# Performance work log

Hardware: AMD Instinct MI355X
Metric: run time of the kernel (lower is better)

The kernel has to match this reference:

```python
import jax, jax.numpy as jnp
import numpy as np

WS = 8      # window_size
NH = 4      # num_heads
DM = 128    # d_model
DK = DM // NH


def _rel_pos_index(ws):
    # matches compute_relative_position_index (static, numpy)
    coords = np.stack(np.meshgrid(np.arange(ws), np.arange(ws), indexing='ij'))  # (2,ws,ws)
    cf = coords.reshape(2, -1)                       # (2, ws*ws)
    rel = (cf[:, :, None] - cf[:, None, :]).transpose(1, 2, 0)  # (S,S,2)
    rel[..., 0] += ws - 1
    rel[..., 1] += ws - 1
    rel[..., 0] *= 2 * ws - 1
    return rel.sum(-1)                               # (S,S) int


def _attn_mask(H, W, ws, ss):
    # matches create_attention_mask (static, numpy)
    row = np.broadcast_to(np.arange(H)[:, None], (H, W))
    col = np.broadcast_to(np.arange(W)[None, :], (H, W))
    wid = row // ws * (W // ws) + col // ws
    wid = np.roll(wid, (-ss, -ss), axis=(0, 1))
    wid = wid.reshape(H // ws, ws, W // ws, ws).transpose(0, 2, 1, 3).reshape(-1, ws * ws)
    return (wid[:, :, None] != wid[:, None, :]).astype(np.float32) * -100.0  # (nw,S,S)


def setup_inputs() -> dict:
    key = jax.random.key(0)
    ks = jax.random.split(key, 10)
    B, N = 16, 128 * 128
    w = lambda k, s: jax.random.normal(k, s, jnp.float32) * 0.02
    return {
        "x": jax.random.normal(ks[0], (B, N, DM), jnp.float32),
        "wq": w(ks[1], (DM, DM)), "bq": jnp.zeros((DM,), jnp.float32),
        "wk": w(ks[2], (DM, DM)), "bk": jnp.zeros((DM,), jnp.float32),
        "wv": w(ks[3], (DM, DM)), "bv": jnp.zeros((DM,), jnp.float32),
        "wo": w(ks[4], (DM, DM)), "bo": jnp.zeros((DM,), jnp.float32),
        "bias_table": w(ks[5], ((2 * WS - 1) ** 2, NH)),
        "shift": 1,
    }


def reference(x, wq, bq, wk, bk, wv, bv, wo, bo, bias_table, shift):
    B, N, C = x.shape
    H = W = int(round(N ** 0.5))
    S = WS * WS
    nw_h, nw_w = H // WS, W // WS
    nw = nw_h * nw_w

    # relative position bias: (NH, S, S)
    rel_idx = _rel_pos_index(WS).reshape(-1)
    bias = bias_table[rel_idx].reshape(S, S, NH).transpose(2, 0, 1)

    xi = x.reshape(B, H, W, C)
    if shift:
        xi = jnp.roll(xi, ((-WS) // 2, (-WS) // 2), axis=(1, 2))

    # window partition -> (B*nw, S, C)
    xw = xi.reshape(B, nw_h, WS, nw_w, WS, C).transpose(0, 1, 3, 2, 4, 5).reshape(B * nw, S, C)

    def proj(w_, b_):
        return (xw @ w_ + b_).reshape(B * nw, S, NH, DK).transpose(0, 2, 1, 3)  # (Bn,NH,S,DK)

    q, k, v = proj(wq, bq), proj(wk, bk), proj(wv, bv)

    scores = jnp.einsum('bhnd,bhmd->bhnm', q, k) / jnp.sqrt(jnp.float32(DK))
    if shift:
        mask = jnp.asarray(_attn_mask(H, W, WS, WS // 2))  # (nw,S,S)
        scores = (scores.reshape(B, nw, NH, S, S) + mask[None, :, None]).reshape(B * nw, NH, S, S)
    scores = scores + bias[None]

    attn = jax.nn.softmax(scores, axis=-1)
    out = jnp.einsum('bhnm,bhmd->bhnd', attn, v)          # (Bn,NH,S,DK)
    out = out.transpose(0, 2, 1, 3).reshape(B * nw, S, DM)
    return out @ wo + bo                                   # (B*nw, S, DM)
```

## Files before the change

### kernel.cpp

```cpp
#include <hip/hip_runtime.h>


typedef __attribute__((ext_vector_type(8))) short bf16x8;
typedef __attribute__((ext_vector_type(4))) float f32x4;

#define MFMA16(a, b, c) __builtin_amdgcn_mfma_f32_16x16x32_bf16((a), (b), (c), 0, 0, 0)

__device__ __forceinline__ unsigned short f2bf(float f) {
  union { float f; unsigned int u; } v; v.f = f;
  unsigned int r = v.u + 0x7fffu + ((v.u >> 16) & 1u);
  return (unsigned short)(r >> 16);
}

__device__ __forceinline__ bf16x8 pack8(f32x4 a, f32x4 b) {
  bf16x8 r;
  r[0] = (short)f2bf(a[0]); r[1] = (short)f2bf(a[1]);
  r[2] = (short)f2bf(a[2]); r[3] = (short)f2bf(a[3]);
  r[4] = (short)f2bf(b[0]); r[5] = (short)f2bf(b[1]);
  r[6] = (short)f2bf(b[2]); r[7] = (short)f2bf(b[3]);
  return r;
}

__global__ void prep_kernel(const float* __restrict__ wq, const float* __restrict__ wk,
                            const float* __restrict__ wv, const float* __restrict__ wo,
                            const float* __restrict__ bias_table,
                            unsigned short* __restrict__ wt, float* __restrict__ bias_full) {
  int tid = blockIdx.x * 256 + threadIdx.x;
  int m = tid >> 14, idx = tid & 16383;
  int n = idx >> 7, k = idx & 127;
  const float* w = (m == 0) ? wq : (m == 1) ? wk : (m == 2) ? wv : wo;
  wt[m * 16384 + n * 128 + k] = f2bf(w[k * 128 + n]);
  if (tid < 16384) {
    int h = tid >> 12, r = tid & 4095;
    int s1 = r >> 6, s2 = r & 63;
    int rel = ((s1 >> 3) - (s2 >> 3) + 7) * 15 + ((s1 & 7) - (s2 & 7) + 7);
    bias_full[tid] = bias_table[rel * 4 + h];
  }
}

__global__ __launch_bounds__(256, 3) void winattn_kernel(
    const float* __restrict__ x,
    const float* __restrict__ bq, const float* __restrict__ bk,
    const float* __restrict__ bv, const float* __restrict__ bo,
    const unsigned short* __restrict__ wt,
    const float* __restrict__ bias_full,
    const int* __restrict__ shiftp,
    float* __restrict__ out) {
  __shared__ __align__(16) char smem[16384];
  const int tid = threadIdx.x;
  const int h = tid >> 6, lane = tid & 63;
  const int g = lane >> 4, c16 = lane & 15;
  const int win = blockIdx.x;
  const int bb = win >> 8, widx = win & 255;
  const int wh = widx >> 4, ww = widx & 15;
  const int shift = shiftp[0];
  const int ss = shift ? 4 : 0;

#pragma unroll
  for (int it = 0; it < 4; ++it) {
    int cid = tid + it * 256;
    int s = cid >> 4, cc = (cid & 15) << 3;
    int r0 = (wh * 8 + (s >> 3) + ss) & 127;
    int c0 = (ww * 8 + (s & 7) + ss) & 127;
    const float* src = x + ((bb * 16384 + r0 * 128 + c0) * 128 + cc);
    float4 lo = *(const float4*)src;
    float4 hi = *(const float4*)(src + 4);
    bf16x8 v;
    v[0] = (short)f2bf(lo.x); v[1] = (short)f2bf(lo.y);
    v[2] = (short)f2bf(lo.z); v[3] = (short)f2bf(lo.w);
    v[4] = (short)f2bf(hi.x); v[5] = (short)f2bf(hi.y);
    v[6] = (short)f2bf(hi.z); v[7] = (short)f2bf(hi.w);
    *(bf16x8*)(smem + s * 256 + ((cc * 2) ^ ((s & 7) << 4))) = v;
  }
  __syncthreads();

  const f32x4 z4 = {0.f, 0.f, 0.f, 0.f};

  f32x4 qacc[2][4], kacc[2][4], vacc[4][2];
#pragma unroll
  for (int i = 0; i < 4; ++i) {
    qacc[0][i] = z4; qacc[1][i] = z4;
    kacc[0][i] = z4; kacc[1][i] = z4;
    vacc[i][0] = z4; vacc[i][1] = z4;
  }
  const unsigned short* wq_ = wt + (h * 32 + c16) * 128;
  const unsigned short* wk_ = wt + 16384 + (h * 32 + c16) * 128;
  const unsigned short* wv_ = wt + 32768 + (h * 32 + c16) * 128;
#pragma unroll
  for (int kk = 0; kk < 4; ++kk) {
    const int co = kk * 32 + g * 8;
    bf16x8 xfr[4];
#pragma unroll
    for (int t = 0; t < 4; ++t) {
      int row = t * 16 + c16;
      xfr[t] = *(const bf16x8*)(smem + row * 256 + ((co * 2) ^ ((row & 7) << 4)));
    }
    bf16x8 wqf0 = *(const bf16x8*)(wq_ + co);
    bf16x8 wqf1 = *(const bf16x8*)(wq_ + 2048 + co);
    bf16x8 wkf0 = *(const bf16x8*)(wk_ + co);
    bf16x8 wkf1 = *(const bf16x8*)(wk_ + 2048 + co);
    bf16x8 wvf0 = *(const bf16x8*)(wv_ + co);
    bf16x8 wvf1 = *(const bf16x8*)(wv_ + 2048 + co);
#pragma unroll
    for (int t = 0; t < 4; ++t) {
      qacc[0][t] = MFMA16(wqf0, xfr[t], qacc[0][t]);
      qacc[1][t] = MFMA16(wqf1, xfr[t], qacc[1][t]);
      kacc[0][t] = MFMA16(wkf0, xfr[t], kacc[0][t]);
      kacc[1][t] = MFMA16(wkf1, xfr[t], kacc[1][t]);
      vacc[t][0] = MFMA16(xfr[t], wvf0, vacc[t][0]);
      vacc[t][1] = MFMA16(xfr[t], wvf1, vacc[t][1]);
    }
  }

  bf16x8 qb16[4], kb16[4], vb16[2][2];
  {
    const float scale = 0.17677669529663687f;
    f32x4 bq4[2], bk4[2];
    bq4[0] = *(const f32x4*)(bq + h * 32 + g * 4);
    bq4[1] = *(const f32x4*)(bq + h * 32 + 16 + g * 4);
    bk4[0] = *(const f32x4*)(bk + h * 32 + g * 4);
    bk4[1] = *(const f32x4*)(bk + h * 32 + 16 + g * 4);
#pragma unroll
    for (int t = 0; t < 4; ++t) {
      f32x4 q0, q1, k0, k1;
#pragma unroll
      for (int r = 0; r < 4; ++r) {
        q0[r] = (qacc[0][t][r] + bq4[0][r]) * scale;
        q1[r] = (qacc[1][t][r] + bq4[1][r]) * scale;
        k0[r] = kacc[0][t][r] + bk4[0][r];
        k1[r] = kacc[1][t][r] + bk4[1][r];
      }
      qb16[t] = pack8(q0, q1);
      kb16[t] = pack8(k0, k1);
    }
    float bv0 = bv[h * 32 + c16];
    float bv1 = bv[h * 32 + 16 + c16];
#pragma unroll
    for (int ks = 0; ks < 2; ++ks) {
      f32x4 v00, v10, v01, v11;
#pragma unroll
      for (int r = 0; r < 4; ++r) {
        v00[r] = vacc[2 * ks][0][r] + bv0;
        v10[r] = vacc[2 * ks + 1][0][r] + bv0;
        v01[r] = vacc[2 * ks][1][r] + bv1;
        v11[r] = vacc[2 * ks + 1][1][r] + bv1;
      }
      vb16[ks][0] = pack8(v00, v10);
      vb16[ks][1] = pack8(v01, v11);
    }
  }

  f32x4 sc[4][4];
#pragma unroll
  for (int a = 0; a < 4; ++a)
#pragma unroll
    for (int b = 0; b < 4; ++b) sc[a][b] = MFMA16(kb16[a], qb16[b], z4);

  int w1i[4] = {0, 0, 0, 0};
  int w2i[4][4] = {};
  if (shift) {
#pragma unroll
    for (int b = 0; b < 4; ++b) {
      int s1 = b * 16 + c16;
      int r0 = (wh * 8 + (s1 >> 3) + ss) & 127;
      int c0 = (ww * 8 + (s1 & 7) + ss) & 127;
      w1i[b] = (r0 >> 3) * 16 + (c0 >> 3);
    }
#pragma unroll
    for (int a = 0; a < 4; ++a)
#pragma unroll
      for (int r = 0; r < 4; ++r) {
        int s2 = a * 16 + g * 4 + r;
        int r0 = (wh * 8 + (s2 >> 3) + ss) & 127;
        int c0 = (ww * 8 + (s2 & 7) + ss) & 127;
        w2i[a][r] = (r0 >> 3) * 16 + (c0 >> 3);
      }
  }

  bf16x8 pa[4][2];
  const float* bfh = bias_full + h * 4096 + c16 * 64 + g * 4;
#pragma unroll
  for (int b = 0; b < 4; ++b) {
    const float* bfr = bfh + b * 1024;
    f32x4 bia[4];
#pragma unroll
    for (int a = 0; a < 4; ++a) bia[a] = *(const f32x4*)(bfr + a * 16);
    float mx = -1e30f;
#pragma unroll
    for (int a = 0; a < 4; ++a)
#pragma unroll
      for (int r = 0; r < 4; ++r) {
        float v = sc[a][b][r] + bia[a][r];
        if (shift && (w1i[b] != w2i[a][r])) v -= 100.f;
        sc[a][b][r] = v;
        mx = fmaxf(mx, v);
      }
    mx = fmaxf(mx, __shfl_xor(mx, 16));
    mx = fmaxf(mx, __shfl_xor(mx, 32));
    float sum = 0.f;
#pragma unroll
    for (int a = 0; a < 4; ++a)
#pragma unroll
      for (int r = 0; r < 4; ++r) {
        float e = __expf(sc[a][b][r] - mx);
        sc[a][b][r] = e;
        sum += e;
      }
    sum += __shfl_xor(sum, 16);
    sum += __shfl_xor(sum, 32);
    float inv = 1.0f / sum;
#pragma unroll
    for (int a = 0; a < 4; ++a)
#pragma unroll
      for (int r = 0; r < 4; ++r) sc[a][b][r] *= inv;
    pa[b][0] = pack8(sc[0][b], sc[1][b]);
    pa[b][1] = pack8(sc[2][b], sc[3][b]);
  }

  f32x4 o[4][2];
#pragma unroll
  for (int b = 0; b < 4; ++b) { o[b][0] = z4; o[b][1] = z4; }
#pragma unroll
  for (int b = 0; b < 4; ++b)
#pragma unroll
    for (int ks = 0; ks < 2; ++ks) {
      o[b][0] = MFMA16(pa[b][ks], vb16[ks][0], o[b][0]);
      o[b][1] = MFMA16(pa[b][ks], vb16[ks][1], o[b][1]);
    }

  __syncthreads();

#pragma unroll
  for (int b = 0; b < 4; ++b)
#pragma unroll
    for (int nt = 0; nt < 2; ++nt)
#pragma unroll
      for (int r = 0; r < 4; ++r) {
        int row = b * 16 + g * 4 + r;
        int col = h * 32 + nt * 16 + c16;
        *(unsigned short*)(smem + row * 256 + ((col * 2) ^ ((row & 7) << 4))) =
            f2bf(o[b][nt][r]);
      }
  __syncthreads();

  {
    f32x4 acc[8];
#pragma unroll
    for (int nt = 0; nt < 8; ++nt) acc[nt] = z4;
    const int arow = h * 16 + c16;
    const int asw = (arow & 7) << 4;
#pragma unroll
    for (int kk = 0; kk < 4; ++kk) {
      const int co = kk * 32 + g * 8;
      bf16x8 a = *(const bf16x8*)(smem + arow * 256 + ((co * 2) ^ asw));
#pragma unroll
      for (int nt = 0; nt < 8; ++nt) {
        bf16x8 bfr = *(const bf16x8*)(wt + 49152 + (nt * 16 + c16) * 128 + co);
        acc[nt] = MFMA16(a, bfr, acc[nt]);
      }
    }
#pragma unroll
    for (int nt = 0; nt < 8; ++nt) {
      int n = nt * 16 + c16;
      float bn = bo[n];
#pragma unroll
      for (int r = 0; r < 4; ++r) {
        int row = h * 16 + g * 4 + r;
        out[(size_t)win * 8192 + (size_t)(row * 128 + n)] = acc[nt][r] + bn;
      }
    }
  }
}

extern "C" void kernel_launch(void* const* d_in, const int* in_sizes, int n_in,
                              void* d_out, int out_size, void* d_ws, size_t ws_size,
                              hipStream_t stream) {
  const float* x = (const float*)d_in[0];
  const float* wq = (const float*)d_in[1];
  const float* bq = (const float*)d_in[2];
  const float* wk = (const float*)d_in[3];
  const float* bk = (const float*)d_in[4];
  const float* wv = (const float*)d_in[5];
  const float* bv = (const float*)d_in[6];
  const float* wo = (const float*)d_in[7];
  const float* bo = (const float*)d_in[8];
  const float* bias_table = (const float*)d_in[9];
  const int* shiftp = (const int*)d_in[10];

  unsigned short* wt = (unsigned short*)d_ws;
  float* bias_full = (float*)((char*)d_ws + 131072);

  prep_kernel<<<256, 256, 0, stream>>>(wq, wk, wv, wo, bias_table, wt, bias_full);
  winattn_kernel<<<4096, 256, 0, stream>>>(x, bq, bk, bv, bo, wt, bias_full, shiftp,
                                           (float*)d_out);
}
```

Measured before the change: 190.9 us.

## Process two windows per block with register-prefetched next window input

Each block now handles two windows, starting the global loads of the second window's input into registers while the first window's attention runs, then converting and storing them into a separate LDS region. This aims to hide global load latency behind compute. It also uses the hardware packed bf16 convert instruction, folds log2(e) into the Q scale and bias table so softmax can use exp2, and raises launch bounds to 4 blocks per CU. The cost is twice the LDS per block, extra live registers for the prefetch, and half as many blocks in the grid.

```diff
diff --git a/kernel.cpp b/kernel.cpp
--- a/kernel.cpp
+++ b/kernel.cpp
@@ -5,20 +5,31 @@
 typedef __attribute__((ext_vector_type(4))) float f32x4;
 
 #define MFMA16(a, b, c) __builtin_amdgcn_mfma_f32_16x16x32_bf16((a), (b), (c), 0, 0, 0)
-
-__device__ __forceinline__ unsigned short f2bf(float f) {
-  union { float f; unsigned int u; } v; v.f = f;
-  unsigned int r = v.u + 0x7fffu + ((v.u >> 16) & 1u);
-  return (unsigned short)(r >> 16);
-}
-
+#define EXP2F(x) __builtin_amdgcn_exp2f(x)
+
+#define XW_OFF 0
+#define STG_OFF 16384
+#define LDS_BYTES 32768
+
+__device__ __forceinline__ unsigned int cvt_pk(float lo, float hi) {
+  unsigned int r;
+  asm("v_cvt_pk_bf16_f32 %0, %1, %2" : "=v"(r) : "v"(lo), "v"(hi));
+  return r;
+}
+__device__ __forceinline__ unsigned short f2bf1(float f) {
+  return (unsigned short)(cvt_pk(f, f) & 0xffffu);
+}
 __device__ __forceinline__ bf16x8 pack8(f32x4 a, f32x4 b) {
-  bf16x8 r;
-  r[0] = (short)f2bf(a[0]); r[1] = (short)f2bf(a[1]);
-  r[2] = (short)f2bf(a[2]); r[3] = (short)f2bf(a[3]);
-  r[4] = (short)f2bf(b[0]); r[5] = (short)f2bf(b[1]);
-  r[6] = (short)f2bf(b[2]); r[7] = (short)f2bf(b[3]);
-  return r;
+  union { unsigned int w[4]; bf16x8 v; } u;
+  u.w[0] = cvt_pk(a[0], a[1]); u.w[1] = cvt_pk(a[2], a[3]);
+  u.w[2] = cvt_pk(b[0], b[1]); u.w[3] = cvt_pk(b[2], b[3]);
+  return u.v;
+}
+__device__ __forceinline__ bf16x8 packf4(float4 lo, float4 hi) {
+  union { unsigned int w[4]; bf16x8 v; } u;
+  u.w[0] = cvt_pk(lo.x, lo.y); u.w[1] = cvt_pk(lo.z, lo.w);
+  u.w[2] = cvt_pk(hi.x, hi.y); u.w[3] = cvt_pk(hi.z, hi.w);
+  return u.v;
 }
 
 __global__ void prep_kernel(const float* __restrict__ wq, const float* __restrict__ wk,
@@ -29,16 +40,28 @@
   int m = tid >> 14, idx = tid & 16383;
   int n = idx >> 7, k = idx & 127;
   const float* w = (m == 0) ? wq : (m == 1) ? wk : (m == 2) ? wv : wo;
-  wt[m * 16384 + n * 128 + k] = f2bf(w[k * 128 + n]);
+  wt[m * 16384 + n * 128 + k] = f2bf1(w[k * 128 + n]);
   if (tid < 16384) {
     int h = tid >> 12, r = tid & 4095;
     int s1 = r >> 6, s2 = r & 63;
     int rel = ((s1 >> 3) - (s2 >> 3) + 7) * 15 + ((s1 & 7) - (s2 & 7) + 7);
-    bias_full[tid] = bias_table[rel * 4 + h];
+    bias_full[tid] = bias_table[rel * 4 + h] * 1.4426950408889634f;
   }
 }
 
-__global__ __launch_bounds__(256, 3) void winattn_kernel(
+__device__ __forceinline__ const float* gsrc(const float* __restrict__ x, int bb, int wh,
+                                             int ww, int ss, int cid) {
+  int s = cid >> 4, cc = (cid & 15) << 3;
+  int r0 = (wh * 8 + (s >> 3) + ss) & 127;
+  int c0 = (ww * 8 + (s & 7) + ss) & 127;
+  return x + ((bb * 16384 + r0 * 128 + c0) * 128 + cc);
+}
+__device__ __forceinline__ void store_xw(char* smem, int cid, bf16x8 v) {
+  int s = cid >> 4, cc = (cid & 15) << 3;
+  *(bf16x8*)(smem + XW_OFF + s * 256 + ((cc * 2) ^ ((s & 7) << 4))) = v;
+}
+
+__global__ __launch_bounds__(256, 4) void winattn_kernel(
     const float* __restrict__ x,
     const float* __restrict__ bq, const float* __restrict__ bk,
     const float* __restrict__ bv, const float* __restrict__ bo,
@@ -46,227 +69,255 @@
     const float* __restrict__ bias_full,
     const int* __restrict__ shiftp,
     float* __restrict__ out) {
-  __shared__ __align__(16) char smem[16384];
+  __shared__ __align__(16) char smem[LDS_BYTES];
   const int tid = threadIdx.x;
   const int h = tid >> 6, lane = tid & 63;
   const int g = lane >> 4, c16 = lane & 15;
-  const int win = blockIdx.x;
-  const int bb = win >> 8, widx = win & 255;
-  const int wh = widx >> 4, ww = widx & 15;
   const int shift = shiftp[0];
   const int ss = shift ? 4 : 0;
-
-#pragma unroll
-  for (int it = 0; it < 4; ++it) {
-    int cid = tid + it * 256;
-    int s = cid >> 4, cc = (cid & 15) << 3;
-    int r0 = (wh * 8 + (s >> 3) + ss) & 127;
-    int c0 = (ww * 8 + (s & 7) + ss) & 127;
-    const float* src = x + ((bb * 16384 + r0 * 128 + c0) * 128 + cc);
-    float4 lo = *(const float4*)src;
-    float4 hi = *(const float4*)(src + 4);
-    bf16x8 v;
-    v[0] = (short)f2bf(lo.x); v[1] = (short)f2bf(lo.y);
-    v[2] = (short)f2bf(lo.z); v[3] = (short)f2bf(lo.w);
-    v[4] = (short)f2bf(hi.x); v[5] = (short)f2bf(hi.y);
-    v[6] = (short)f2bf(hi.z); v[7] = (short)f2bf(hi.w);
-    *(bf16x8*)(smem + s * 256 + ((cc * 2) ^ ((s & 7) << 4))) = v;
+  const f32x4 z4 = {0.f, 0.f, 0.f, 0.f};
+
+  const int win0 = blockIdx.x, win1 = blockIdx.x + 2048;
+  const int bb1 = win1 >> 8, wh1 = (win1 >> 4) & 15, ww1 = win1 & 15;
+
+  {
+    const int bb0 = win0 >> 8, wh0 = (win0 >> 4) & 15, ww0 = win0 & 15;
+#pragma unroll
+    for (int it = 0; it < 4; ++it) {
+      int cid = tid + it * 256;
+      const float* src = gsrc(x, bb0, wh0, ww0, ss, cid);
+      float4 lo = *(const float4*)src;
+      float4 hi = *(const float4*)(src + 4);
+      store_xw(smem, cid, packf4(lo, hi));
+    }
   }
-  __syncthreads();
-
-  const f32x4 z4 = {0.f, 0.f, 0.f, 0.f};
-
-  f32x4 qacc[2][4], kacc[2][4], vacc[4][2];
-#pragma unroll
-  for (int i = 0; i < 4; ++i) {
-    qacc[0][i] = z4; qacc[1][i] = z4;
-    kacc[0][i] = z4; kacc[1][i] = z4;
-    vacc[i][0] = z4; vacc[i][1] = z4;
+  float4 pre0[4], pre1[4];
+  {
+    const float* s0 = gsrc(x, bb1, wh1, ww1, ss, tid);
+    const float* s1 = gsrc(x, bb1, wh1, ww1, ss, tid + 256);
+    pre0[0] = *(const float4*)s0; pre0[1] = *(const float4*)(s0 + 4);
+    pre0[2] = *(const float4*)s1; pre0[3] = *(const float4*)(s1 + 4);
   }
-  const unsigned short* wq_ = wt + (h * 32 + c16) * 128;
-  const unsigned short* wk_ = wt + 16384 + (h * 32 + c16) * 128;
-  const unsigned short* wv_ = wt + 32768 + (h * 32 + c16) * 128;
-#pragma unroll
-  for (int kk = 0; kk < 4; ++kk) {
-    const int co = kk * 32 + g * 8;
-    bf16x8 xfr[4];
-#pragma unroll
-    for (int t = 0; t < 4; ++t) {
-      int row = t * 16 + c16;
-      xfr[t] = *(const bf16x8*)(smem + row * 256 + ((co * 2) ^ ((row & 7) << 4)));
-    }
-    bf16x8 wqf0 = *(const bf16x8*)(wq_ + co);
-    bf16x8 wqf1 = *(const bf16x8*)(wq_ + 2048 + co);
-    bf16x8 wkf0 = *(const bf16x8*)(wk_ + co);
-    bf16x8 wkf1 = *(const bf16x8*)(wk_ + 2048 + co);
-    bf16x8 wvf0 = *(const bf16x8*)(wv_ + co);
-    bf16x8 wvf1 = *(const bf16x8*)(wv_ + 2048 + co);
-#pragma unroll
-    for (int t = 0; t < 4; ++t) {
-      qacc[0][t] = MFMA16(wqf0, xfr[t], qacc[0][t]);
-      qacc[1][t] = MFMA16(wqf1, xfr[t], qacc[1][t]);
-      kacc[0][t] = MFMA16(wkf0, xfr[t], kacc[0][t]);
-      kacc[1][t] = MFMA16(wkf1, xfr[t], kacc[1][t]);
-      vacc[t][0] = MFMA16(xfr[t], wvf0, vacc[t][0]);
-      vacc[t][1] = MFMA16(xfr[t], wvf1, vacc[t][1]);
-    }
-  }
-
-  bf16x8 qb16[4], kb16[4], vb16[2][2];
-  {
-    const float scale = 0.17677669529663687f;
-    f32x4 bq4[2], bk4[2];
-    bq4[0] = *(const f32x4*)(bq + h * 32 + g * 4);
-    bq4[1] = *(const f32x4*)(bq + h * 32 + 16 + g * 4);
-    bk4[0] = *(const f32x4*)(bk + h * 32 + g * 4);
-    bk4[1] = *(const f32x4*)(bk + h * 32 + 16 + g * 4);
-#pragma unroll
-    for (int t = 0; t < 4; ++t) {
-      f32x4 q0, q1, k0, k1;
-#pragma unroll
-      for (int r = 0; r < 4; ++r) {
-        q0[r] = (qacc[0][t][r] + bq4[0][r]) * scale;
-        q1[r] = (qacc[1][t][r] + bq4[1][r]) * scale;
-        k0[r] = kacc[0][t][r] + bk4[0][r];
-        k1[r] = kacc[1][t][r] + bk4[1][r];
-      }
-      qb16[t] = pack8(q0, q1);
-      kb16[t] = pack8(k0, k1);
-    }
-    float bv0 = bv[h * 32 + c16];
-    float bv1 = bv[h * 32 + 16 + c16];
-#pragma unroll
-    for (int ks = 0; ks < 2; ++ks) {
-      f32x4 v00, v10, v01, v11;
-#pragma unroll
-      for (int r = 0; r < 4; ++r) {
-        v00[r] = vacc[2 * ks][0][r] + bv0;
-        v10[r] = vacc[2 * ks + 1][0][r] + bv0;
-        v01[r] = vacc[2 * ks][1][r] + bv1;
-        v11[r] = vacc[2 * ks + 1][1][r] + bv1;
-      }
-      vb16[ks][0] = pack8(v00, v10);
-      vb16[ks][1] = pack8(v01, v11);
-    }
-  }
-
-  f32x4 sc[4][4];
-#pragma unroll
-  for (int a = 0; a < 4; ++a)
-#pragma unroll
-    for (int b = 0; b < 4; ++b) sc[a][b] = MFMA16(kb16[a], qb16[b], z4);
-
-  int w1i[4] = {0, 0, 0, 0};
-  int w2i[4][4] = {};
-  if (shift) {
-#pragma unroll
-    for (int b = 0; b < 4; ++b) {
-      int s1 = b * 16 + c16;
-      int r0 = (wh * 8 + (s1 >> 3) + ss) & 127;
-      int c0 = (ww * 8 + (s1 & 7) + ss) & 127;
-      w1i[b] = (r0 >> 3) * 16 + (c0 >> 3);
-    }
-#pragma unroll
-    for (int a = 0; a < 4; ++a)
-#pragma unroll
-      for (int r = 0; r < 4; ++r) {
-        int s2 = a * 16 + g * 4 + r;
-        int r0 = (wh * 8 + (s2 >> 3) + ss) & 127;
-        int c0 = (ww * 8 + (s2 & 7) + ss) & 127;
-        w2i[a][r] = (r0 >> 3) * 16 + (c0 >> 3);
-      }
-  }
-
-  bf16x8 pa[4][2];
-  const float* bfh = bias_full + h * 4096 + c16 * 64 + g * 4;
-#pragma unroll
-  for (int b = 0; b < 4; ++b) {
-    const float* bfr = bfh + b * 1024;
-    f32x4 bia[4];
-#pragma unroll
-    for (int a = 0; a < 4; ++a) bia[a] = *(const f32x4*)(bfr + a * 16);
-    float mx = -1e30f;
-#pragma unroll
-    for (int a = 0; a < 4; ++a)
-#pragma unroll
-      for (int r = 0; r < 4; ++r) {
-        float v = sc[a][b][r] + bia[a][r];
-        if (shift && (w1i[b] != w2i[a][r])) v -= 100.f;
-        sc[a][b][r] = v;
-        mx = fmaxf(mx, v);
-      }
-    mx = fmaxf(mx, __shfl_xor(mx, 16));
-    mx = fmaxf(mx, __shfl_xor(mx, 32));
-    float sum = 0.f;
-#pragma unroll
-    for (int a = 0; a < 4; ++a)
-#pragma unroll
-      for (int r = 0; r < 4; ++r) {
-        float e = __expf(sc[a][b][r] - mx);
-        sc[a][b][r] = e;
-        sum += e;
-      }
-    sum += __shfl_xor(sum, 16);
-    sum += __shfl_xor(sum, 32);
-    float inv = 1.0f / sum;
-#pragma unroll
-    for (int a = 0; a < 4; ++a)
-#pragma unroll
-      for (int r = 0; r < 4; ++r) sc[a][b][r] *= inv;
-    pa[b][0] = pack8(sc[0][b], sc[1][b]);
-    pa[b][1] = pack8(sc[2][b], sc[3][b]);
-  }
-
-  f32x4 o[4][2];
-#pragma unroll
-  for (int b = 0; b < 4; ++b) { o[b][0] = z4; o[b][1] = z4; }
-#pragma unroll
-  for (int b = 0; b < 4; ++b)
-#pragma unroll
-    for (int ks = 0; ks < 2; ++ks) {
-      o[b][0] = MFMA16(pa[b][ks], vb16[ks][0], o[b][0]);
-      o[b][1] = MFMA16(pa[b][ks], vb16[ks][1], o[b][1]);
-    }
-
-  __syncthreads();
-
-#pragma unroll
-  for (int b = 0; b < 4; ++b)
-#pragma unroll
-    for (int nt = 0; nt < 2; ++nt)
-#pragma unroll
-      for (int r = 0; r < 4; ++r) {
-        int row = b * 16 + g * 4 + r;
-        int col = h * 32 + nt * 16 + c16;
-        *(unsigned short*)(smem + row * 256 + ((col * 2) ^ ((row & 7) << 4))) =
-            f2bf(o[b][nt][r]);
-      }
-  __syncthreads();
-
-  {
-    f32x4 acc[8];
-#pragma unroll
-    for (int nt = 0; nt < 8; ++nt) acc[nt] = z4;
-    const int arow = h * 16 + c16;
-    const int asw = (arow & 7) << 4;
+
+  for (int w = 0; w < 2; ++w) {
+    const int win = w ? win1 : win0;
+    const int wh = (win >> 4) & 15, ww = win & 15;
+    __syncthreads();
+
+    f32x4 qacc[2][4], kacc[2][4], vacc[4][2];
+#pragma unroll
+    for (int i = 0; i < 4; ++i) {
+      qacc[0][i] = z4; qacc[1][i] = z4;
+      kacc[0][i] = z4; kacc[1][i] = z4;
+      vacc[i][0] = z4; vacc[i][1] = z4;
+    }
+    const unsigned short* wq_ = wt + (h * 32 + c16) * 128;
+    const unsigned short* wk_ = wt + 16384 + (h * 32 + c16) * 128;
+    const unsigned short* wv_ = wt + 32768 + (h * 32 + c16) * 128;
 #pragma unroll
     for (int kk = 0; kk < 4; ++kk) {
       const int co = kk * 32 + g * 8;
-      bf16x8 a = *(const bf16x8*)(smem + arow * 256 + ((co * 2) ^ asw));
+      bf16x8 xfr[4];
+#pragma unroll
+      for (int t = 0; t < 4; ++t) {
+        int row = t * 16 + c16;
+        xfr[t] = *(const bf16x8*)(smem + XW_OFF + row * 256 + ((co * 2) ^ ((row & 7) << 4)));
+      }
+      bf16x8 wqf0 = *(const bf16x8*)(wq_ + co);
+      bf16x8 wqf1 = *(const bf16x8*)(wq_ + 2048 + co);
+      bf16x8 wkf0 = *(const bf16x8*)(wk_ + co);
+      bf16x8 wkf1 = *(const bf16x8*)(wk_ + 2048 + co);
+      bf16x8 wvf0 = *(const bf16x8*)(wv_ + co);
+      bf16x8 wvf1 = *(const bf16x8*)(wv_ + 2048 + co);
+#pragma unroll
+      for (int t = 0; t < 4; ++t) {
+        qacc[0][t] = MFMA16(wqf0, xfr[t], qacc[0][t]);
+        qacc[1][t] = MFMA16(wqf1, xfr[t], qacc[1][t]);
+        kacc[0][t] = MFMA16(wkf0, xfr[t], kacc[0][t]);
+        kacc[1][t] = MFMA16(wkf1, xfr[t], kacc[1][t]);
+        vacc[t][0] = MFMA16(xfr[t], wvf0, vacc[t][0]);
+        vacc[t][1] = MFMA16(xfr[t], wvf1, vacc[t][1]);
+      }
+    }
+
+    bf16x8 qb16[4], kb16[4], vb16[2][2];
+    {
+      const float scale = 0.17677669529663687f * 1.4426950408889634f;
+      f32x4 bq4[2], bk4[2];
+      bq4[0] = *(const f32x4*)(bq + h * 32 + g * 4);
+      bq4[1] = *(const f32x4*)(bq + h * 32 + 16 + g * 4);
+      bk4[0] = *(const f32x4*)(bk + h * 32 + g * 4);
+      bk4[1] = *(const f32x4*)(bk + h * 32 + 16 + g * 4);
+#pragma unroll
+      for (int t = 0; t < 4; ++t) {
+        f32x4 q0, q1, k0, k1;
+#pragma unroll
+        for (int r = 0; r < 4; ++r) {
+          q0[r] = (qacc[0][t][r] + bq4[0][r]) * scale;
+          q1[r] = (qacc[1][t][r] + bq4[1][r]) * scale;
+          k0[r] = kacc[0][t][r] + bk4[0][r];
+          k1[r] = kacc[1][t][r] + bk4[1][r];
+        }
+        qb16[t] = pack8(q0, q1);
+        kb16[t] = pack8(k0, k1);
+      }
+      float bv0 = bv[h * 32 + c16];
+      float bv1 = bv[h * 32 + 16 + c16];
+#pragma unroll
+      for (int ks = 0; ks < 2; ++ks) {
+        f32x4 v00, v10, v01, v11;
+#pragma unroll
+        for (int r = 0; r < 4; ++r) {
+          v00[r] = vacc[2 * ks][0][r] + bv0;
+          v10[r] = vacc[2 * ks + 1][0][r] + bv0;
+          v01[r] = vacc[2 * ks][1][r] + bv1;
+          v11[r] = vacc[2 * ks + 1][1][r] + bv1;
+        }
+        vb16[ks][0] = pack8(v00, v10);
+        vb16[ks][1] = pack8(v01, v11);
+      }
+    }
+
+    f32x4 sc[4][4];
+#pragma unroll
+    for (int a = 0; a < 4; ++a)
+#pragma unroll
+      for (int b = 0; b < 4; ++b) sc[a][b] = MFMA16(kb16[a], qb16[b], z4);
+
+    int w1i[4] = {0, 0, 0, 0};
+    int w2i[4][4] = {};
+    if (shift) {
+#pragma unroll
+      for (int b = 0; b < 4; ++b) {
+        int s1 = b * 16 + c16;
+        int r0 = (wh * 8 + (s1 >> 3) + ss) & 127;
+        int c0 = (ww * 8 + (s1 & 7) + ss) & 127;
+        w1i[b] = (r0 >> 3) * 16 + (c0 >> 3);
+      }
+#pragma unroll
+      for (int a = 0; a < 4; ++a)
+#pragma unroll
+        for (int r = 0; r < 4; ++r) {
+          int s2 = a * 16 + g * 4 + r;
+          int r0 = (wh * 8 + (s2 >> 3) + ss) & 127;
+          int c0 = (ww * 8 + (s2 & 7) + ss) & 127;
+          w2i[a][r] = (r0 >> 3) * 16 + (c0 >> 3);
+        }
+    }
+
+    bf16x8 pa[4][2];
+    const float* bfh = bias_full + h * 4096 + c16 * 64 + g * 4;
+#pragma unroll
+    for (int b = 0; b < 4; ++b) {
+      const float* bfr = bfh + b * 1024;
+      f32x4 bia[4];
+#pragma unroll
+      for (int a = 0; a < 4; ++a) bia[a] = *(const f32x4*)(bfr + a * 16);
+#pragma unroll
+      for (int a = 0; a < 4; ++a)
+#pragma unroll
+        for (int r = 0; r < 4; ++r) {
+          float v = sc[a][b][r] + bia[a][r];
+          if (shift && (w1i[b] != w2i[a][r])) v -= 144.2695040888963f;
+          sc[a][b][r] = v;
+        }
+      f32x4 m01, m23;
+#pragma unroll
+      for (int r = 0; r < 4; ++r) {
+        m01[r] = fmaxf(sc[0][b][r], sc[1][b][r]);
+        m23[r] = fmaxf(sc[2][b][r], sc[3][b][r]);
+      }
+      float mx = fmaxf(fmaxf(fmaxf(m01[0], m01[1]), fmaxf(m01[2], m01[3])),
+                       fmaxf(fmaxf(m23[0], m23[1]), fmaxf(m23[2], m23[3])));
+      mx = fmaxf(mx, __shfl_xor(mx, 16));
+      mx = fmaxf(mx, __shfl_xor(mx, 32));
+#pragma unroll
+      for (int a = 0; a < 4; ++a)
+#pragma unroll
+        for (int r = 0; r < 4; ++r) sc[a][b][r] = EXP2F(sc[a][b][r] - mx);
+      f32x4 s01, s23;
+#pragma unroll
+      for (int r = 0; r < 4; ++r) {
+        s01[r] = sc[0][b][r] + sc[1][b][r];
+        s23[r] = sc[2][b][r] + sc[3][b][r];
+      }
+      float sum = ((s01[0] + s01[1]) + (s01[2] + s01[3])) +
+                  ((s23[0] + s23[1]) + (s23[2] + s23[3]));
+      sum += __shfl_xor(sum, 16);
+      sum += __shfl_xor(sum, 32);
+      float inv = 1.0f / sum;
+#pragma unroll
+      for (int a = 0; a < 4; ++a)
+#pragma unroll
+        for (int r = 0; r < 4; ++r) sc[a][b][r] *= inv;
+      pa[b][0] = pack8(sc[0][b], sc[1][b]);
+      pa[b][1] = pack8(sc[2][b], sc[3][b]);
+    }
+
+    if (w == 0) {
+      const float* s2p = gsrc(x, bb1, wh1, ww1, ss, tid + 512);
+      const float* s3p = gsrc(x, bb1, wh1, ww1, ss, tid + 768);
+      pre1[0] = *(const float4*)s2p; pre1[1] = *(const float4*)(s2p + 4);
+      pre1[2] = *(const float4*)s3p; pre1[3] = *(const float4*)(s3p + 4);
+    }
+
+    f32x4 o[4][2];
+#pragma unroll
+    for (int b = 0; b < 4; ++b) { o[b][0] = z4; o[b][1] = z4; }
+#pragma unroll
+    for (int b = 0; b < 4; ++b)
+#pragma unroll
+      for (int ks = 0; ks < 2; ++ks) {
+        o[b][0] = MFMA16(pa[b][ks], vb16[ks][0], o[b][0]);
+        o[b][1] = MFMA16(pa[b][ks], vb16[ks][1], o[b][1]);
+      }
+
+    __syncthreads();
+
+    if (w == 0) {
+      store_xw(smem, tid,       packf4(pre0[0], pre0[1]));
+      store_xw(smem, tid + 256, packf4(pre0[2], pre0[3]));
+      store_xw(smem, tid + 512, packf4(pre1[0], pre1[1]));
+      store_xw(smem, tid + 768, packf4(pre1[2], pre1[3]));
+    }
+#pragma unroll
+    for (int b = 0; b < 4; ++b)
+#pragma unroll
+      for (int nt = 0; nt < 2; ++nt)
+#pragma unroll
+        for (int r = 0; r < 4; ++r) {
+          int row = b * 16 + g * 4 + r;
+          int col = h * 32 + nt * 16 + c16;
+          *(unsigned short*)(smem + STG_OFF + row * 256 + ((col * 2) ^ ((row & 7) << 4))) =
+              f2bf1(o[b][nt][r]);
+        }
+    __syncthreads();
+
+    {
+      f32x4 acc[8];
+#pragma unroll
+      for (int nt = 0; nt < 8; ++nt) acc[nt] = z4;
+      const int arow = h * 16 + c16;
+      const int asw = (arow & 7) << 4;
+#pragma unroll
+      for (int kk = 0; kk < 4; ++kk) {
+        const int co = kk * 32 + g * 8;
+        bf16x8 a = *(const bf16x8*)(smem + STG_OFF + arow * 256 + ((co * 2) ^ asw));
+#pragma unroll
+        for (int nt = 0; nt < 8; ++nt) {
+          bf16x8 bfr = *(const bf16x8*)(wt + 49152 + (nt * 16 + c16) * 128 + co);
+          acc[nt] = MFMA16(a, bfr, acc[nt]);
+        }
+      }
 #pragma unroll
       for (int nt = 0; nt < 8; ++nt) {
-        bf16x8 bfr = *(const bf16x8*)(wt + 49152 + (nt * 16 + c16) * 128 + co);
-        acc[nt] = MFMA16(a, bfr, acc[nt]);
-      }
-    }
-#pragma unroll
-    for (int nt = 0; nt < 8; ++nt) {
-      int n = nt * 16 + c16;
-      float bn = bo[n];
-#pragma unroll
-      for (int r = 0; r < 4; ++r) {
-        int row = h * 16 + g * 4 + r;
-        out[(size_t)win * 8192 + (size_t)(row * 128 + n)] = acc[nt][r] + bn;
+        int n = nt * 16 + c16;
+        float bn = bo[n];
+#pragma unroll
+        for (int r = 0; r < 4; ++r) {
+          int row = h * 16 + g * 4 + r;
+          out[(size_t)win * 8192 + (size_t)(row * 128 + n)] = acc[nt][r] + bn;
+        }
       }
     }
   }
@@ -291,6 +342,6 @@
   float* bias_full = (float*)((char*)d_ws + 131072);
 
   prep_kernel<<<256, 256, 0, stream>>>(wq, wk, wv, wo, bias_table, wt, bias_full);
-  winattn_kernel<<<4096, 256, 0, stream>>>(x, bq, bk, bv, bo, wt, bias_full, shiftp,
+  winattn_kernel<<<2048, 256, 0, stream>>>(x, bq, bk, bv, bo, wt, bias_full, shiftp,
                                            (float*)d_out);
 }
```

Measured after the change: 654.8 us. +243.0%, slower.
